# Kernel tuning notes

Measured on AMD Instinct MI355X. Metric: run time of the kernel, lower is better.

## Reference

```python
import jax, jax.numpy as jnp
import numpy as np

POOL_SIZE = (14, 14)  # from init_kwargs


def setup_inputs() -> dict:
    key = jax.random.key(0)
    k1, k2 = jax.random.split(key)
    feature = jax.random.normal(k1, (1, 50, 50, 1024), dtype=jnp.float32)
    # rois in original-image coordinates [y1, x1, y2, x2], image is 800x800
    raw = jax.random.uniform(k2, (512, 4), dtype=jnp.float32) * 800.0
    y1 = jnp.minimum(raw[:, 0], raw[:, 2])
    y2 = jnp.maximum(raw[:, 0], raw[:, 2])
    x1 = jnp.minimum(raw[:, 1], raw[:, 3])
    x2 = jnp.maximum(raw[:, 1], raw[:, 3])
    rois = jnp.stack([y1, x1, y2, x2], axis=1)
    img_size = jnp.array([800, 800], dtype=jnp.int32)
    return {"feature": feature, "rois": rois, "img_size": img_size}


def _crop_and_resize(image, boxes, crop_size):
    """Faithful jax port of tf.image.crop_and_resize (bilinear, single image,
    all box_ind == 0). image: [1,H,W,C]; boxes: [N,4] normalized [y1,x1,y2,x2]."""
    H, W = image.shape[1], image.shape[2]
    ch, cw = crop_size
    img = image[0]  # [H, W, C]
    y1, x1, y2, x2 = boxes[:, 0], boxes[:, 1], boxes[:, 2], boxes[:, 3]
    # Sample grid in source-image pixel coordinates (TF convention: corners map
    # to box corners scaled by (dim-1)).
    ty = jnp.arange(ch, dtype=boxes.dtype) / (ch - 1)  # [ch]
    tx = jnp.arange(cw, dtype=boxes.dtype) / (cw - 1)  # [cw]
    ys = (y1[:, None] + ty[None, :] * (y2 - y1)[:, None]) * (H - 1)  # [N, ch]
    xs = (x1[:, None] + tx[None, :] * (x2 - x1)[:, None]) * (W - 1)  # [N, cw]
    y0f = jnp.floor(ys)
    x0f = jnp.floor(xs)
    wy = ys - y0f  # [N, ch] bilinear weights
    wx = xs - x0f  # [N, cw]
    y0 = jnp.clip(y0f, 0, H - 1).astype(jnp.int32)
    y1i = jnp.clip(y0f + 1, 0, H - 1).astype(jnp.int32)
    x0 = jnp.clip(x0f, 0, W - 1).astype(jnp.int32)
    x1i = jnp.clip(x0f + 1, 0, W - 1).astype(jnp.int32)

    def gather(yi, xi):  # [N,ch],[N,cw] -> [N,ch,cw,C]
        return img[yi[:, :, None], xi[:, None, :]]

    wxb = wx[:, None, :, None]  # [N,1,cw,1]
    wyb = wy[:, :, None, None]  # [N,ch,1,1]
    top = gather(y0, x0) * (1.0 - wxb) + gather(y0, x1i) * wxb
    bot = gather(y1i, x0) * (1.0 - wxb) + gather(y1i, x1i) * wxb
    return top * (1.0 - wyb) + bot * wyb  # [N, ch, cw, C]


def reference(feature, rois, img_size):
    h = img_size[0].astype(jnp.float32)
    w = img_size[1].astype(jnp.float32)
    normalization = jnp.stack([h, w, h, w], axis=0)
    boxes = rois / normalization
    return _crop_and_resize(feature, boxes, POOL_SIZE)
```

## Files before the change

### kernel.cpp

```cpp
#include <hip/hip_runtime.h>


#define FH 50
#define FW 50
#define FC 1024
#define PH 14
#define PW 14
#define CS 64
#define NSL (FC / CS)
#define QS (CS / 4)
#define COLPAD 17

typedef float f32x4 __attribute__((ext_vector_type(4)));

__global__ __launch_bounds__(256) void roi_crop_resize_kernel(
    const float* __restrict__ feat,
    const float* __restrict__ rois,
    const int* __restrict__ img_size,
    float* __restrict__ out)
{
    __shared__ f32x4 lds[2][FW][COLPAD];

    int bid = blockIdx.x;
    int n = bid >> 4;
    int s = bid & (NSL - 1);
    int t = threadIdx.x;

    float hs = (float)img_size[0];
    float ws = (float)img_size[1];
    float by1 = rois[n * 4 + 0] / hs;
    float bx1 = rois[n * 4 + 1] / ws;
    float by2 = rois[n * 4 + 2] / hs;
    float bx2 = rois[n * 4 + 3] / ws;

    float ybase = by1 * (float)(FH - 1);
    float dy    = (by2 - by1) * (float)(FH - 1) * (1.0f / (float)(PH - 1));
    float xbase = bx1 * (float)(FW - 1);
    float dxs   = (bx2 - bx1) * (float)(FW - 1) * (1.0f / (float)(PW - 1));

    int xlo  = (int)floorf(xbase);
    int xhi  = min((int)floorf(xbase + (float)(PW - 1) * dxs) + 1, FW - 1);
    int ncol = xhi - xlo + 1;

    int q = t & 15;
    int j = t >> 4;
    float wx = 0.0f; int c0l = 0, c1l = 0;
    if (j < PW) {
        float xs  = xbase + (float)j * dxs;
        float x0f = floorf(xs);
        wx = xs - x0f;
        int x0 = (int)x0f;
        int x1 = min(x0 + 1, FW - 1);
        c0l = x0 - xlo;
        c1l = x1 - xlo;
    }

    const f32x4* featq = (const f32x4*)feat;
    int sq = s * QS;

    int Lst = -1000;

    for (int i = 0; i < PH; ++i) {
        float ysf = ybase + (float)i * dy;
        float y0f = floorf(ysf);
        float wy  = ysf - y0f;
        int r0 = (int)y0f;
        int r1 = min(r0 + 1, FH - 1);

        int start = max(Lst + 1, r0);
        if (start <= r1) {
            __syncthreads();
            for (int r = start; r <= r1; ++r) {
                f32x4* dst = &lds[r & 1][0][0];
                int base = (r * FW + xlo) * (FC / 4) + sq;
                for (int e = t; e < ncol * QS; e += 256) {
                    int col = e >> 4;
                    int qq  = e & 15;
                    dst[col * COLPAD + qq] = featq[base + col * (FC / 4) + qq];
                }
            }
            Lst = r1;
            __syncthreads();
        }

        if (j < PW) {
            const f32x4* rT = &lds[r0 & 1][0][0];
            const f32x4* rB = &lds[r1 & 1][0][0];
            f32x4 a = rT[c0l * COLPAD + q];
            f32x4 b = rT[c1l * COLPAD + q];
            f32x4 c = rB[c0l * COLPAD + q];
            f32x4 d = rB[c1l * COLPAD + q];
            float omwx = 1.0f - wx;
            float omwy = 1.0f - wy;
            f32x4 res = (a * omwx + b * wx) * omwy + (c * omwx + d * wx) * wy;
            f32x4* o = (f32x4*)out + ((n * (PH * PW) + i * PW + j) * (FC / 4) + sq + q);
            __builtin_nontemporal_store(res, o);
        }
    }
}

extern "C" void kernel_launch(void* const* d_in, const int* in_sizes, int n_in,
                              void* d_out, int out_size, void* d_ws, size_t ws_size,
                              hipStream_t stream) {
    const float* feat     = (const float*)d_in[0];
    const float* rois     = (const float*)d_in[1];
    const int*   img_size = (const int*)d_in[2];
    float* out = (float*)d_out;

    int n_rois = in_sizes[1] / 4;
    int grid   = n_rois * NSL;

    roi_crop_resize_kernel<<<grid, 256, 0, stream>>>(feat, rois, img_size, out);
}
```

Baseline: 85.37 us.

## Replace LDS row staging with direct global gathers and unroll the row loop

Removes the shared-memory staging of feature rows and the __syncthreads barriers, so each thread now gathers its four bilinear corner vectors straight from global memory (relying on L2/L1 for reuse). The output-row loop is fully unrolled so loads from different rows can be in flight at once. The cost is more global/L1 traffic, since overlapping rows and columns are re-read instead of shared through LDS. Index clamping is now done in float before the int conversion.

```diff
diff --git a/kernel.cpp b/kernel.cpp
--- a/kernel.cpp
+++ b/kernel.cpp
@@ -9,7 +9,6 @@
 #define CS 64
 #define NSL (FC / CS)
 #define QS (CS / 4)
-#define COLPAD 17
 
 typedef float f32x4 __attribute__((ext_vector_type(4)));
 
@@ -19,12 +18,12 @@
     const int* __restrict__ img_size,
     float* __restrict__ out)
 {
-    __shared__ f32x4 lds[2][FW][COLPAD];
-
     int bid = blockIdx.x;
     int n = bid >> 4;
     int s = bid & (NSL - 1);
     int t = threadIdx.x;
+    int q = t & 15;
+    int j = t >> 4;
 
     float hs = (float)img_size[0];
     float ws = (float)img_size[1];
@@ -38,63 +37,39 @@
     float xbase = bx1 * (float)(FW - 1);
     float dxs   = (bx2 - bx1) * (float)(FW - 1) * (1.0f / (float)(PW - 1));
 
-    int xlo  = (int)floorf(xbase);
-    int xhi  = min((int)floorf(xbase + (float)(PW - 1) * dxs) + 1, FW - 1);
-    int ncol = xhi - xlo + 1;
+    float xs  = xbase + (float)j * dxs;
+    float x0f = floorf(xs);
+    float wx  = xs - x0f;
+    int x0 = (int)fminf(fmaxf(x0f,        0.0f), (float)(FW - 1));
+    int x1 = (int)fminf(fmaxf(x0f + 1.0f, 0.0f), (float)(FW - 1));
+    float omwx = 1.0f - wx;
 
-    int q = t & 15;
-    int j = t >> 4;
-    float wx = 0.0f; int c0l = 0, c1l = 0;
-    if (j < PW) {
-        float xs  = xbase + (float)j * dxs;
-        float x0f = floorf(xs);
-        wx = xs - x0f;
-        int x0 = (int)x0f;
-        int x1 = min(x0 + 1, FW - 1);
-        c0l = x0 - xlo;
-        c1l = x1 - xlo;
-    }
+    const f32x4* fq = (const f32x4*)feat;
+    int sq = s * QS + q;
+    f32x4* ob = (f32x4*)out + ((size_t)n * (PH * PW)) * (FC / 4) + sq;
 
-    const f32x4* featq = (const f32x4*)feat;
-    int sq = s * QS;
+    bool active = (j < PW);
 
-    int Lst = -1000;
-
+    #pragma unroll
     for (int i = 0; i < PH; ++i) {
         float ysf = ybase + (float)i * dy;
         float y0f = floorf(ysf);
         float wy  = ysf - y0f;
-        int r0 = (int)y0f;
-        int r1 = min(r0 + 1, FH - 1);
+        int r0 = (int)fminf(fmaxf(y0f,        0.0f), (float)(FH - 1));
+        int r1 = (int)fminf(fmaxf(y0f + 1.0f, 0.0f), (float)(FH - 1));
+        float omwy = 1.0f - wy;
 
-        int start = max(Lst + 1, r0);
-        if (start <= r1) {
-            __syncthreads();
-            for (int r = start; r <= r1; ++r) {
-                f32x4* dst = &lds[r & 1][0][0];
-                int base = (r * FW + xlo) * (FC / 4) + sq;
-                for (int e = t; e < ncol * QS; e += 256) {
-                    int col = e >> 4;
-                    int qq  = e & 15;
-                    dst[col * COLPAD + qq] = featq[base + col * (FC / 4) + qq];
-                }
-            }
-            Lst = r1;
-            __syncthreads();
-        }
+        if (active) {
+            int bT = (r0 * FW) * (FC / 4) + sq;
+            int bB = (r1 * FW) * (FC / 4) + sq;
+            f32x4 a = fq[bT + x0 * (FC / 4)];
+            f32x4 b = fq[bT + x1 * (FC / 4)];
+            f32x4 c = fq[bB + x0 * (FC / 4)];
+            f32x4 d = fq[bB + x1 * (FC / 4)];
 
-        if (j < PW) {
-            const f32x4* rT = &lds[r0 & 1][0][0];
-            const f32x4* rB = &lds[r1 & 1][0][0];
-            f32x4 a = rT[c0l * COLPAD + q];
-            f32x4 b = rT[c1l * COLPAD + q];
-            f32x4 c = rB[c0l * COLPAD + q];
-            f32x4 d = rB[c1l * COLPAD + q];
-            float omwx = 1.0f - wx;
-            float omwy = 1.0f - wy;
             f32x4 res = (a * omwx + b * wx) * omwy + (c * omwx + d * wx) * wy;
-            f32x4* o = (f32x4*)out + ((n * (PH * PW) + i * PW + j) * (FC / 4) + sq + q);
-            __builtin_nontemporal_store(res, o);
+
+            __builtin_nontemporal_store(res, ob + (i * PW + j) * (FC / 4));
         }
     }
 }
```

Measured after the change: 80.71 us. -5.5%, faster.
